# Optimization experiments

Measured on AMD Instinct MI355X. Metric: run time of the kernel, lower is better.

The kernel has to match this reference:

```python
import jax, jax.numpy as jnp
import numpy as np

N, D, E = 40000, 128, 640000
ALPHA = 0.1   # GCNII alpha
BETA = 1.0    # GCN2Conv theta=None => beta = 1.0
BN_EPS = 1e-5


def setup_inputs() -> dict:
    key = jax.random.key(0)
    ks = jax.random.split(key, 5)
    x = jax.random.normal(ks[0], (N, D), jnp.float32)
    x_orig = jax.random.normal(ks[1], (N, D), jnp.float32)
    edge_index = jax.random.randint(ks[2], (2, E), 0, N, dtype=jnp.int64)
    edge_weights = jax.random.uniform(ks[3], (E,), jnp.float32)
    W = jax.random.normal(ks[4], (D, D), jnp.float32) / np.sqrt(D).astype(np.float32)
    gamma = jnp.ones((D,), jnp.float32)
    beta = jnp.zeros((D,), jnp.float32)
    return dict(x=x, x_orig=x_orig, edge_index=edge_index,
                edge_weights=edge_weights, W=W, gamma=gamma, beta=beta)


def _gcn_norm(edge_index, edge_weight, num_nodes):
    # PyG gcn_norm: add self loops (weight 1), symmetric D^{-1/2} A D^{-1/2}
    loop = jnp.arange(num_nodes, dtype=edge_index.dtype)
    row = jnp.concatenate([edge_index[0], loop])   # source
    col = jnp.concatenate([edge_index[1], loop])   # target
    ew = jnp.concatenate([edge_weight, jnp.ones((num_nodes,), edge_weight.dtype)])
    deg = jax.ops.segment_sum(ew, col, num_segments=num_nodes)
    dis = jnp.where(deg > 0, jax.lax.rsqrt(deg), 0.0)
    norm = dis[row] * ew * dis[col]
    return row, col, norm


def reference(x, x_orig, edge_index, edge_weights, W, gamma, beta):
    n = x.shape[0]
    row, col, norm = _gcn_norm(edge_index, edge_weights, n)
    # sparse neighbor aggregation: gather x[row], scale, scatter-add to col
    agg = jax.ops.segment_sum(norm[:, None] * x[row], col, num_segments=n)
    # GCNII initial-residual blend; theta=None => out = blended @ W (beta=1)
    h = ((1.0 - ALPHA) * agg + ALPHA * x_orig) @ W
    h = jax.nn.relu(h)
    # BatchNorm1d (training mode: batch statistics, biased variance)
    mean = h.mean(axis=0)
    var = h.var(axis=0)
    h = (h - mean) * jax.lax.rsqrt(var + BN_EPS) * gamma + beta
    return h
```

## Files before the change

### kernel.cpp

```cpp
#include <hip/hip_runtime.h>

#define NN 40000
#define DD 128
#define EE 640000

__global__ __launch_bounds__(256) void k_init(int* __restrict__ cnt,
                                              float* __restrict__ sums) {
    int i = blockIdx.x * 256 + threadIdx.x;
    if (i < NN) cnt[i] = 0;
    if (i < 256) sums[i] = 0.0f;
}

__global__ __launch_bounds__(256) void k_rank(const int* __restrict__ ei,
                                              int* __restrict__ cnt,
                                              int* __restrict__ rank) {
    int e = blockIdx.x * 256 + threadIdx.x;
    int c = ei[EE + e];
    rank[e] = atomicAdd(&cnt[c], 1);
}

#define SCAN_CH 40
__global__ __launch_bounds__(1024) void k_scan(const int* __restrict__ cnt,
                                               int* __restrict__ off) {
    __shared__ int sm[1024];
    int t = threadIdx.x;
    int base = t * SCAN_CH;
    int s = 0;
    if (base < NN) {
#pragma unroll
        for (int i = 0; i < SCAN_CH; ++i) s += cnt[base + i];
    }
    sm[t] = s;
    __syncthreads();
    for (int d = 1; d < 1024; d <<= 1) {
        int v = (t >= d) ? sm[t - d] : 0;
        __syncthreads();
        sm[t] += v;
        __syncthreads();
    }
    if (base < NN) {
        int run = sm[t] - s;
#pragma unroll
        for (int i = 0; i < SCAN_CH; ++i) {
            off[base + i] = run;
            run += cnt[base + i];
        }
    }
    if (t == 1023) off[NN] = sm[1023];
}

__global__ __launch_bounds__(256) void k_permute(const int* __restrict__ ei,
                                                 const float* __restrict__ ew,
                                                 const int* __restrict__ rank,
                                                 const int* __restrict__ off,
                                                 int2* __restrict__ srn) {
    int e = blockIdx.x * 256 + threadIdx.x;
    int r = ei[e], c = ei[EE + e];
    int pos = off[c] + rank[e];
    srn[pos] = make_int2(r, __float_as_int(ew[e]));
}

__global__ __launch_bounds__(256) void k_degdis(const int* __restrict__ off,
                                                const int2* __restrict__ srn,
                                                float* __restrict__ dis) {
    int gid = blockIdx.x * 256 + threadIdx.x;
    int node = gid >> 6;
    int lane = gid & 63;
    int s = off[node], e = off[node + 1];
    float v = 0.0f;
    for (int p = s + lane; p < e; p += 64) v += __int_as_float(srn[p].y);
#pragma unroll
    for (int m = 1; m < 64; m <<= 1) v += __shfl_xor(v, m);
    if (lane == 0) dis[node] = rsqrtf(1.0f + v);
}

__global__ __launch_bounds__(256) void k_gather(const int* __restrict__ off,
                                                const int2* __restrict__ srn,
                                                const float* __restrict__ x,
                                                const float* __restrict__ dis,
                                                float* __restrict__ agg) {
    int gid = blockIdx.x * 256 + threadIdx.x;
    int node = gid >> 6;
    int lane = gid & 63;
    const float2* x2 = (const float2*)x;
    float dc = dis[node];
    float2 sv = x2[(size_t)node * 64 + lane];
    float2 acc0 = {sv.x * dc, sv.y * dc};
    float2 acc1 = {0.f, 0.f}, acc2 = {0.f, 0.f}, acc3 = {0.f, 0.f};
    int s = off[node], e_end = off[node + 1];
    for (int bse = s; bse < e_end; bse += 64) {
        int ee = bse + lane;
        bool act = (ee < e_end);
        int2 rv = act ? srn[ee] : make_int2(0, 0);
        float dl = act ? dis[rv.x] : 0.0f;
        float nmL = __int_as_float(rv.y) * dl;
        int nb = min(64, e_end - bse);
        int j = 0;
        for (; j + 4 <= nb; j += 4) {
            int r0 = __shfl(rv.x, j);
            int r1 = __shfl(rv.x, j + 1);
            int r2 = __shfl(rv.x, j + 2);
            int r3 = __shfl(rv.x, j + 3);
            float n0 = __shfl(nmL, j);
            float n1 = __shfl(nmL, j + 1);
            float n2 = __shfl(nmL, j + 2);
            float n3 = __shfl(nmL, j + 3);
            float2 v0 = x2[(size_t)r0 * 64 + lane];
            float2 v1 = x2[(size_t)r1 * 64 + lane];
            float2 v2 = x2[(size_t)r2 * 64 + lane];
            float2 v3 = x2[(size_t)r3 * 64 + lane];
            acc0.x = fmaf(n0, v0.x, acc0.x); acc0.y = fmaf(n0, v0.y, acc0.y);
            acc1.x = fmaf(n1, v1.x, acc1.x); acc1.y = fmaf(n1, v1.y, acc1.y);
            acc2.x = fmaf(n2, v2.x, acc2.x); acc2.y = fmaf(n2, v2.y, acc2.y);
            acc3.x = fmaf(n3, v3.x, acc3.x); acc3.y = fmaf(n3, v3.y, acc3.y);
        }
        for (; j < nb; ++j) {
            int rr = __shfl(rv.x, j);
            float nm = __shfl(nmL, j);
            float2 v = x2[(size_t)rr * 64 + lane];
            acc0.x = fmaf(nm, v.x, acc0.x); acc0.y = fmaf(nm, v.y, acc0.y);
        }
    }
    acc0.x = dc * (acc0.x + acc1.x + acc2.x + acc3.x);
    acc0.y = dc * (acc0.y + acc1.y + acc2.y + acc3.y);
    ((float2*)agg)[(size_t)node * 64 + lane] = acc0;
}

__global__ __launch_bounds__(256) void k_matmul(const float* __restrict__ agg,
                                                const float* __restrict__ xorig,
                                                const float* __restrict__ W,
                                                float* __restrict__ out) {
    __shared__ float Wl[DD * DD];
    int t = threadIdx.x;
    {
        const float4* Wg = (const float4*)W;
        float4* Wl4 = (float4*)Wl;
#pragma unroll
        for (int i = 0; i < 16; ++i) Wl4[i * 256 + t] = Wg[i * 256 + t];
    }
    __syncthreads();

    int rl = t >> 2, jg = t & 3;
    int r0 = blockIdx.x * 256 + rl * 4;
    bool valid = (r0 + 3) < NN;
    size_t rr = valid ? (size_t)r0 : 0;
    int j0 = jg * 32;
    int jg2 = jg * 2;

    float4 acc[4][8] = {};
    const float* ap = agg + rr * DD;
    const float* bp = xorig + rr * DD;

    for (int k0 = 0; k0 < DD; k0 += 4) {
        float in[4][4];
#pragma unroll
        for (int r = 0; r < 4; ++r) {
            float4 av = *(const float4*)(ap + r * DD + k0);
            float4 bv = *(const float4*)(bp + r * DD + k0);
            in[r][0] = 0.9f * av.x + 0.1f * bv.x;
            in[r][1] = 0.9f * av.y + 0.1f * bv.y;
            in[r][2] = 0.9f * av.z + 0.1f * bv.z;
            in[r][3] = 0.9f * av.w + 0.1f * bv.w;
        }
#pragma unroll
        for (int kk = 0; kk < 4; ++kk) {
            const float* wr = &Wl[(k0 + kk) * DD + j0];
#pragma unroll
            for (int mp = 0; mp < 8; ++mp) {
                float4 w = *(const float4*)(wr + ((jg2 + mp) & 7) * 4);
#pragma unroll
                for (int r = 0; r < 4; ++r) {
                    acc[r][mp].x = fmaf(in[r][kk], w.x, acc[r][mp].x);
                    acc[r][mp].y = fmaf(in[r][kk], w.y, acc[r][mp].y);
                    acc[r][mp].z = fmaf(in[r][kk], w.z, acc[r][mp].z);
                    acc[r][mp].w = fmaf(in[r][kk], w.w, acc[r][mp].w);
                }
            }
        }
    }
    if (valid) {
#pragma unroll
        for (int r = 0; r < 4; ++r) {
            float* orow = out + (rr + r) * DD;
#pragma unroll
            for (int mp = 0; mp < 8; ++mp) {
                int cm = j0 + ((jg2 + mp) & 7) * 4;
                float4 v = acc[r][mp];
                v.x = fmaxf(v.x, 0.0f);
                v.y = fmaxf(v.y, 0.0f);
                v.z = fmaxf(v.z, 0.0f);
                v.w = fmaxf(v.w, 0.0f);
                *(float4*)(orow + cm) = v;
            }
        }
    }
}

__global__ __launch_bounds__(256) void k_stats(const float* __restrict__ h,
                                               float* __restrict__ sums) {
    int t = threadIdx.x;
    int tid = blockIdx.x * 256 + t;
    int cg = t & 31;
    int row0 = tid >> 5;
    float4 s = {0, 0, 0, 0}, q = {0, 0, 0, 0};
    for (int r = row0; r < NN; r += 2048) {
        float4 v = *(const float4*)&h[(size_t)r * DD + cg * 4];
        s.x += v.x; s.y += v.y; s.z += v.z; s.w += v.w;
        q.x += v.x * v.x; q.y += v.y * v.y; q.z += v.z * v.z; q.w += v.w * v.w;
    }
    __shared__ float red[256][8];
    red[t][0] = s.x; red[t][1] = s.y; red[t][2] = s.z; red[t][3] = s.w;
    red[t][4] = q.x; red[t][5] = q.y; red[t][6] = q.z; red[t][7] = q.w;
    __syncthreads();
    if (t < 32) {
#pragma unroll
        for (int s8 = 1; s8 < 8; ++s8)
#pragma unroll
            for (int c = 0; c < 8; ++c) red[t][c] += red[t + 32 * s8][c];
        int j = t * 4;
        unsafeAtomicAdd(&sums[j + 0], red[t][0]);
        unsafeAtomicAdd(&sums[j + 1], red[t][1]);
        unsafeAtomicAdd(&sums[j + 2], red[t][2]);
        unsafeAtomicAdd(&sums[j + 3], red[t][3]);
        unsafeAtomicAdd(&sums[DD + j + 0], red[t][4]);
        unsafeAtomicAdd(&sums[DD + j + 1], red[t][5]);
        unsafeAtomicAdd(&sums[DD + j + 2], red[t][6]);
        unsafeAtomicAdd(&sums[DD + j + 3], red[t][7]);
    }
}

__global__ __launch_bounds__(256) void k_apply(float* __restrict__ h,
                                               const float* __restrict__ sums,
                                               const float* __restrict__ gamma,
                                               const float* __restrict__ beta) {
    int g = blockIdx.x * 256 + threadIdx.x;
    int i = g >> 5, q = g & 31;
    int j = q * 4;
    const float invN = 1.0f / (float)NN;
    float4 sm = *(const float4*)&sums[j];
    float4 sq = *(const float4*)&sums[DD + j];
    float4 gm = *(const float4*)&gamma[j];
    float4 bt = *(const float4*)&beta[j];
    float4 v = *(float4*)&h[(size_t)i * DD + j];
    float m0 = sm.x * invN, m1 = sm.y * invN, m2 = sm.z * invN, m3 = sm.w * invN;
    float i0 = rsqrtf(fmaxf(sq.x * invN - m0 * m0, 0.0f) + 1e-5f);
    float i1 = rsqrtf(fmaxf(sq.y * invN - m1 * m1, 0.0f) + 1e-5f);
    float i2 = rsqrtf(fmaxf(sq.z * invN - m2 * m2, 0.0f) + 1e-5f);
    float i3 = rsqrtf(fmaxf(sq.w * invN - m3 * m3, 0.0f) + 1e-5f);
    v.x = (v.x - m0) * i0 * gm.x + bt.x;
    v.y = (v.y - m1) * i1 * gm.y + bt.y;
    v.z = (v.z - m2) * i2 * gm.z + bt.z;
    v.w = (v.w - m3) * i3 * gm.w + bt.w;
    *(float4*)&h[(size_t)i * DD + j] = v;
}

extern "C" void kernel_launch(void* const* d_in, const int* in_sizes, int n_in,
                              void* d_out, int out_size, void* d_ws, size_t ws_size,
                              hipStream_t stream) {
    const float* x     = (const float*)d_in[0];
    const float* xorig = (const float*)d_in[1];
    const int*   ei    = (const int*)d_in[2];
    const float* ew    = (const float*)d_in[3];
    const float* W     = (const float*)d_in[4];
    const float* gamma = (const float*)d_in[5];
    const float* beta  = (const float*)d_in[6];
    float* out = (float*)d_out;

    float* ws   = (float*)d_ws;
    float* agg  = ws;
    int2*  srn  = (int2*)(agg + (size_t)NN * DD);
    float* dis  = (float*)(srn + EE);
    float* sums = dis + NN;
    int*   cnt  = (int*)(sums + 256);
    int*   off  = cnt + NN;
    int*   rank = off + NN + 1;

    k_init   <<<160,   256, 0, stream>>>(cnt, sums);
    k_rank   <<<2500,  256, 0, stream>>>(ei, cnt, rank);
    k_scan   <<<1,    1024, 0, stream>>>(cnt, off);
    k_permute<<<2500,  256, 0, stream>>>(ei, ew, rank, off, srn);
    k_degdis <<<10000, 256, 0, stream>>>(off, srn, dis);
    k_gather <<<10000, 256, 0, stream>>>(off, srn, x, dis, agg);
    k_matmul <<<157,   256, 0, stream>>>(agg, xorig, W, out);
    k_stats  <<<256,   256, 0, stream>>>(out, sums);
    k_apply  <<<5000,  256, 0, stream>>>(out, sums, gamma, beta);
}
```

Baseline: 284.5 us.

## Restructure matmul to one row per thread with column-split grid

Rewrites the dense blend-matmul kernel so each thread computes one output row over a 32-column slice, with a 2D grid splitting the output columns into four groups. W is no longer staged in LDS; it is read directly from global memory with block-uniform addresses. The goal is more blocks and lighter per-thread register pressure, so the GPU is better occupied than with 157 large-tile blocks. In exchange, agg and x_orig are read four times, and per-thread row-strided loads are less coalesced.

```diff
diff --git a/kernel.cpp b/kernel.cpp
--- a/kernel.cpp
+++ b/kernel.cpp
@@ -130,69 +130,44 @@
                                                 const float* __restrict__ xorig,
                                                 const float* __restrict__ W,
                                                 float* __restrict__ out) {
-    __shared__ float Wl[DD * DD];
-    int t = threadIdx.x;
-    {
-        const float4* Wg = (const float4*)W;
-        float4* Wl4 = (float4*)Wl;
-#pragma unroll
-        for (int i = 0; i < 16; ++i) Wl4[i * 256 + t] = Wg[i * 256 + t];
-    }
-    __syncthreads();
-
-    int rl = t >> 2, jg = t & 3;
-    int r0 = blockIdx.x * 256 + rl * 4;
-    bool valid = (r0 + 3) < NN;
-    size_t rr = valid ? (size_t)r0 : 0;
-    int j0 = jg * 32;
-    int jg2 = jg * 2;
-
-    float4 acc[4][8] = {};
-    const float* ap = agg + rr * DD;
-    const float* bp = xorig + rr * DD;
+    int row = blockIdx.x * 256 + threadIdx.x;
+    if (row >= NN) return;
+    int j0 = blockIdx.y << 5;
+
+    float4 acc[8] = {};
+    const float* ap = agg + (size_t)row * DD;
+    const float* bp = xorig + (size_t)row * DD;
 
     for (int k0 = 0; k0 < DD; k0 += 4) {
-        float in[4][4];
-#pragma unroll
-        for (int r = 0; r < 4; ++r) {
-            float4 av = *(const float4*)(ap + r * DD + k0);
-            float4 bv = *(const float4*)(bp + r * DD + k0);
-            in[r][0] = 0.9f * av.x + 0.1f * bv.x;
-            in[r][1] = 0.9f * av.y + 0.1f * bv.y;
-            in[r][2] = 0.9f * av.z + 0.1f * bv.z;
-            in[r][3] = 0.9f * av.w + 0.1f * bv.w;
-        }
+        float4 av = *(const float4*)(ap + k0);
+        float4 bv = *(const float4*)(bp + k0);
+        float in[4];
+        in[0] = 0.9f * av.x + 0.1f * bv.x;
+        in[1] = 0.9f * av.y + 0.1f * bv.y;
+        in[2] = 0.9f * av.z + 0.1f * bv.z;
+        in[3] = 0.9f * av.w + 0.1f * bv.w;
 #pragma unroll
         for (int kk = 0; kk < 4; ++kk) {
-            const float* wr = &Wl[(k0 + kk) * DD + j0];
+            const float* wr = W + (size_t)(k0 + kk) * DD + j0;
 #pragma unroll
             for (int mp = 0; mp < 8; ++mp) {
-                float4 w = *(const float4*)(wr + ((jg2 + mp) & 7) * 4);
-#pragma unroll
-                for (int r = 0; r < 4; ++r) {
-                    acc[r][mp].x = fmaf(in[r][kk], w.x, acc[r][mp].x);
-                    acc[r][mp].y = fmaf(in[r][kk], w.y, acc[r][mp].y);
-                    acc[r][mp].z = fmaf(in[r][kk], w.z, acc[r][mp].z);
-                    acc[r][mp].w = fmaf(in[r][kk], w.w, acc[r][mp].w);
-                }
+                float4 w = *(const float4*)(wr + mp * 4);
+                acc[mp].x = fmaf(in[kk], w.x, acc[mp].x);
+                acc[mp].y = fmaf(in[kk], w.y, acc[mp].y);
+                acc[mp].z = fmaf(in[kk], w.z, acc[mp].z);
+                acc[mp].w = fmaf(in[kk], w.w, acc[mp].w);
             }
         }
     }
-    if (valid) {
-#pragma unroll
-        for (int r = 0; r < 4; ++r) {
-            float* orow = out + (rr + r) * DD;
-#pragma unroll
-            for (int mp = 0; mp < 8; ++mp) {
-                int cm = j0 + ((jg2 + mp) & 7) * 4;
-                float4 v = acc[r][mp];
-                v.x = fmaxf(v.x, 0.0f);
-                v.y = fmaxf(v.y, 0.0f);
-                v.z = fmaxf(v.z, 0.0f);
-                v.w = fmaxf(v.w, 0.0f);
-                *(float4*)(orow + cm) = v;
-            }
-        }
+    float* orow = out + (size_t)row * DD + j0;
+#pragma unroll
+    for (int mp = 0; mp < 8; ++mp) {
+        float4 v = acc[mp];
+        v.x = fmaxf(v.x, 0.0f);
+        v.y = fmaxf(v.y, 0.0f);
+        v.z = fmaxf(v.z, 0.0f);
+        v.w = fmaxf(v.w, 0.0f);
+        *(float4*)(orow + mp * 4) = v;
     }
 }
 
@@ -281,7 +256,7 @@
     k_permute<<<2500,  256, 0, stream>>>(ei, ew, rank, off, srn);
     k_degdis <<<10000, 256, 0, stream>>>(off, srn, dis);
     k_gather <<<10000, 256, 0, stream>>>(off, srn, x, dis, agg);
-    k_matmul <<<157,   256, 0, stream>>>(agg, xorig, W, out);
+    k_matmul <<<dim3(157, 4), 256, 0, stream>>>(agg, xorig, W, out);
     k_stats  <<<256,   256, 0, stream>>>(out, sums);
     k_apply  <<<5000,  256, 0, stream>>>(out, sums, gamma, beta);
 }
```

Result: slower. 333.5 us (+17.2%).

## Process two nodes per wave in gather and split matmul columns across blocks

Applied to the files above, without the earlier changes.

The gather kernel now assigns two destination nodes per 64-lane wave, with each half-wave loading float4 rows. This halves the grid and widens the per-lane loads, so each wave has more memory requests in flight. The matmul now tiles by 128 rows and 64 output columns over a 313x2 grid, which halves the shared-memory W tile and lets more blocks run across the CUs. The cost is that agg and x_orig rows are read twice, and half-waves whose node has fewer edges sit idle while their partner half loops.

```diff
diff --git a/kernel.cpp b/kernel.cpp
--- a/kernel.cpp
+++ b/kernel.cpp
@@ -80,74 +80,93 @@
                                                 const float* __restrict__ dis,
                                                 float* __restrict__ agg) {
     int gid = blockIdx.x * 256 + threadIdx.x;
-    int node = gid >> 6;
+    int wave = gid >> 6;
     int lane = gid & 63;
-    const float2* x2 = (const float2*)x;
+    int half = lane >> 5;
+    int l32  = lane & 31;
+    int node = wave * 2 + half;
+    int srcb = half << 5;
+    const float4* x4 = (const float4*)x;
+
     float dc = dis[node];
-    float2 sv = x2[(size_t)node * 64 + lane];
-    float2 acc0 = {sv.x * dc, sv.y * dc};
-    float2 acc1 = {0.f, 0.f}, acc2 = {0.f, 0.f}, acc3 = {0.f, 0.f};
-    int s = off[node], e_end = off[node + 1];
-    for (int bse = s; bse < e_end; bse += 64) {
-        int ee = bse + lane;
-        bool act = (ee < e_end);
+    float4 sv = x4[(size_t)node * 32 + l32];
+    float4 acc0 = {sv.x * dc, sv.y * dc, sv.z * dc, sv.w * dc};
+    float4 acc1 = {0, 0, 0, 0}, acc2 = {0, 0, 0, 0}, acc3 = {0, 0, 0, 0};
+
+    int p = off[node], eend = off[node + 1];
+    while (__any(p < eend)) {
+        int ee = p + l32;
+        bool act = ee < eend;
         int2 rv = act ? srn[ee] : make_int2(0, 0);
         float dl = act ? dis[rv.x] : 0.0f;
-        float nmL = __int_as_float(rv.y) * dl;
-        int nb = min(64, e_end - bse);
+        float nm = __int_as_float(rv.y) * dl;
+        int nb = eend - p;
+        nb = nb < 0 ? 0 : (nb > 32 ? 32 : nb);
         int j = 0;
         for (; j + 4 <= nb; j += 4) {
-            int r0 = __shfl(rv.x, j);
-            int r1 = __shfl(rv.x, j + 1);
-            int r2 = __shfl(rv.x, j + 2);
-            int r3 = __shfl(rv.x, j + 3);
-            float n0 = __shfl(nmL, j);
-            float n1 = __shfl(nmL, j + 1);
-            float n2 = __shfl(nmL, j + 2);
-            float n3 = __shfl(nmL, j + 3);
-            float2 v0 = x2[(size_t)r0 * 64 + lane];
-            float2 v1 = x2[(size_t)r1 * 64 + lane];
-            float2 v2 = x2[(size_t)r2 * 64 + lane];
-            float2 v3 = x2[(size_t)r3 * 64 + lane];
+            int r0 = __shfl(rv.x, srcb + j);
+            int r1 = __shfl(rv.x, srcb + j + 1);
+            int r2 = __shfl(rv.x, srcb + j + 2);
+            int r3 = __shfl(rv.x, srcb + j + 3);
+            float n0 = __shfl(nm, srcb + j);
+            float n1 = __shfl(nm, srcb + j + 1);
+            float n2 = __shfl(nm, srcb + j + 2);
+            float n3 = __shfl(nm, srcb + j + 3);
+            float4 v0 = x4[(size_t)r0 * 32 + l32];
+            float4 v1 = x4[(size_t)r1 * 32 + l32];
+            float4 v2 = x4[(size_t)r2 * 32 + l32];
+            float4 v3 = x4[(size_t)r3 * 32 + l32];
             acc0.x = fmaf(n0, v0.x, acc0.x); acc0.y = fmaf(n0, v0.y, acc0.y);
+            acc0.z = fmaf(n0, v0.z, acc0.z); acc0.w = fmaf(n0, v0.w, acc0.w);
             acc1.x = fmaf(n1, v1.x, acc1.x); acc1.y = fmaf(n1, v1.y, acc1.y);
+            acc1.z = fmaf(n1, v1.z, acc1.z); acc1.w = fmaf(n1, v1.w, acc1.w);
             acc2.x = fmaf(n2, v2.x, acc2.x); acc2.y = fmaf(n2, v2.y, acc2.y);
+            acc2.z = fmaf(n2, v2.z, acc2.z); acc2.w = fmaf(n2, v2.w, acc2.w);
             acc3.x = fmaf(n3, v3.x, acc3.x); acc3.y = fmaf(n3, v3.y, acc3.y);
+            acc3.z = fmaf(n3, v3.z, acc3.z); acc3.w = fmaf(n3, v3.w, acc3.w);
         }
         for (; j < nb; ++j) {
-            int rr = __shfl(rv.x, j);
-            float nm = __shfl(nmL, j);
-            float2 v = x2[(size_t)rr * 64 + lane];
-            acc0.x = fmaf(nm, v.x, acc0.x); acc0.y = fmaf(nm, v.y, acc0.y);
-        }
+            int rr = __shfl(rv.x, srcb + j);
+            float nn = __shfl(nm, srcb + j);
+            float4 v = x4[(size_t)rr * 32 + l32];
+            acc0.x = fmaf(nn, v.x, acc0.x); acc0.y = fmaf(nn, v.y, acc0.y);
+            acc0.z = fmaf(nn, v.z, acc0.z); acc0.w = fmaf(nn, v.w, acc0.w);
+        }
+        p += 32;
     }
     acc0.x = dc * (acc0.x + acc1.x + acc2.x + acc3.x);
     acc0.y = dc * (acc0.y + acc1.y + acc2.y + acc3.y);
-    ((float2*)agg)[(size_t)node * 64 + lane] = acc0;
+    acc0.z = dc * (acc0.z + acc1.z + acc2.z + acc3.z);
+    acc0.w = dc * (acc0.w + acc1.w + acc2.w + acc3.w);
+    ((float4*)agg)[(size_t)node * 32 + l32] = acc0;
 }
 
 __global__ __launch_bounds__(256) void k_matmul(const float* __restrict__ agg,
                                                 const float* __restrict__ xorig,
                                                 const float* __restrict__ W,
                                                 float* __restrict__ out) {
-    __shared__ float Wl[DD * DD];
+    __shared__ float Wl[DD * 64];
     int t = threadIdx.x;
+    int jb = blockIdx.y << 6;
     {
-        const float4* Wg = (const float4*)W;
-        float4* Wl4 = (float4*)Wl;
-#pragma unroll
-        for (int i = 0; i < 16; ++i) Wl4[i * 256 + t] = Wg[i * 256 + t];
+#pragma unroll
+        for (int i = 0; i < 8; ++i) {
+            int idx = i * 256 + t;
+            int k = idx >> 4, jq = idx & 15;
+            *(float4*)&Wl[k * 64 + jq * 4] =
+                *(const float4*)&W[(size_t)k * DD + jb + jq * 4];
+        }
     }
     __syncthreads();
 
-    int rl = t >> 2, jg = t & 3;
-    int r0 = blockIdx.x * 256 + rl * 4;
-    bool valid = (r0 + 3) < NN;
-    size_t rr = valid ? (size_t)r0 : 0;
-    int j0 = jg * 32;
-    int jg2 = jg * 2;
-
-    float4 acc[4][8] = {};
+    int rg = t >> 3;
+    int cg = t & 7;
+    int row0 = blockIdx.x * 128 + rg * 4;
+    bool valid = (row0 + 3) < NN;
+    size_t rr = valid ? (size_t)row0 : 0;
+    int jc = cg * 8;
+
+    float acc[4][8] = {};
     const float* ap = agg + rr * DD;
     const float* bp = xorig + rr * DD;
 
@@ -164,34 +183,32 @@
         }
 #pragma unroll
         for (int kk = 0; kk < 4; ++kk) {
-            const float* wr = &Wl[(k0 + kk) * DD + j0];
-#pragma unroll
-            for (int mp = 0; mp < 8; ++mp) {
-                float4 w = *(const float4*)(wr + ((jg2 + mp) & 7) * 4);
-#pragma unroll
-                for (int r = 0; r < 4; ++r) {
-                    acc[r][mp].x = fmaf(in[r][kk], w.x, acc[r][mp].x);
-                    acc[r][mp].y = fmaf(in[r][kk], w.y, acc[r][mp].y);
-                    acc[r][mp].z = fmaf(in[r][kk], w.z, acc[r][mp].z);
-                    acc[r][mp].w = fmaf(in[r][kk], w.w, acc[r][mp].w);
-                }
+            float4 w0 = *(const float4*)&Wl[(k0 + kk) * 64 + jc];
+            float4 w1 = *(const float4*)&Wl[(k0 + kk) * 64 + jc + 4];
+#pragma unroll
+            for (int r = 0; r < 4; ++r) {
+                float a = in[r][kk];
+                acc[r][0] = fmaf(a, w0.x, acc[r][0]);
+                acc[r][1] = fmaf(a, w0.y, acc[r][1]);
+                acc[r][2] = fmaf(a, w0.z, acc[r][2]);
+                acc[r][3] = fmaf(a, w0.w, acc[r][3]);
+                acc[r][4] = fmaf(a, w1.x, acc[r][4]);
+                acc[r][5] = fmaf(a, w1.y, acc[r][5]);
+                acc[r][6] = fmaf(a, w1.z, acc[r][6]);
+                acc[r][7] = fmaf(a, w1.w, acc[r][7]);
             }
         }
     }
     if (valid) {
 #pragma unroll
         for (int r = 0; r < 4; ++r) {
-            float* orow = out + (rr + r) * DD;
-#pragma unroll
-            for (int mp = 0; mp < 8; ++mp) {
-                int cm = j0 + ((jg2 + mp) & 7) * 4;
-                float4 v = acc[r][mp];
-                v.x = fmaxf(v.x, 0.0f);
-                v.y = fmaxf(v.y, 0.0f);
-                v.z = fmaxf(v.z, 0.0f);
-                v.w = fmaxf(v.w, 0.0f);
-                *(float4*)(orow + cm) = v;
-            }
+            float* orow = out + (rr + r) * DD + jb + jc;
+            float4 v0 = {fmaxf(acc[r][0], 0.0f), fmaxf(acc[r][1], 0.0f),
+                         fmaxf(acc[r][2], 0.0f), fmaxf(acc[r][3], 0.0f)};
+            float4 v1 = {fmaxf(acc[r][4], 0.0f), fmaxf(acc[r][5], 0.0f),
+                         fmaxf(acc[r][6], 0.0f), fmaxf(acc[r][7], 0.0f)};
+            *(float4*)(orow) = v0;
+            *(float4*)(orow + 4) = v1;
         }
     }
 }
@@ -280,8 +297,8 @@
     k_scan   <<<1,    1024, 0, stream>>>(cnt, off);
     k_permute<<<2500,  256, 0, stream>>>(ei, ew, rank, off, srn);
     k_degdis <<<10000, 256, 0, stream>>>(off, srn, dis);
-    k_gather <<<10000, 256, 0, stream>>>(off, srn, x, dis, agg);
-    k_matmul <<<157,   256, 0, stream>>>(agg, xorig, W, out);
+    k_gather <<<5000,  256, 0, stream>>>(off, srn, x, dis, agg);
+    k_matmul <<<dim3(313, 2), 256, 0, stream>>>(agg, xorig, W, out);
     k_stats  <<<256,   256, 0, stream>>>(out, sums);
     k_apply  <<<5000,  256, 0, stream>>>(out, sums, gamma, beta);
 }
```

After: 288.3 us. No clear change (+1.3%).
